# Kernel tuning notes

Measured on AMD Instinct MI355X. Metric: run time of the kernel, lower is better.

Reference implementation:

```python
import jax, jax.numpy as jnp
import numpy as np

N = 40000      # nodes
E = 640000     # edges (avg degree 16)
H = 128        # hidden_dim
D = 4          # propagation_depth
G = 1250       # graphs in batch
T = 32         # target_dim
AF, AV = 9, 64   # atom categorical features, vocab per feature
BF, BV = 3, 8    # bond categorical features, vocab per feature


def silu(x):
    return x * jax.nn.sigmoid(x)


def setup_inputs() -> dict:
    key = jax.random.key(0)
    ks = jax.random.split(key, 32)
    s = 1.0 / np.sqrt(H)

    def w(i, shp, scale):
        return (jax.random.normal(ks[i], shp, jnp.float32) * scale).astype(jnp.float32)

    inp = {}
    inp["atom_feat"] = jax.random.randint(ks[0], (N, AF), 0, AV)
    inp["bond_feat"] = jax.random.randint(ks[1], (E, BF), 0, BV)
    inp["edge_src"] = jax.random.randint(ks[2], (E,), 0, N)
    inp["edge_dst"] = jax.random.randint(ks[3], (E,), 0, N)
    inp["node2graph"] = jnp.sort(jax.random.randint(ks[4], (N,), 0, G))

    inp["atom_emb"] = w(5, (AF, AV, H), 0.1)
    inp["bond_emb"] = w(6, (BF, BV, H), 0.1)
    # message MLP: Linear(3H,H)+SiLU, Linear(H,H)+SiLU (last_activation=mid_activation)
    inp["msg_W1"] = w(7, (D, 3 * H, H), 1.0 / np.sqrt(3 * H))
    inp["msg_b1"] = jnp.zeros((D, H), jnp.float32)
    inp["msg_W2"] = w(8, (D, H, H), s)
    inp["msg_b2"] = jnp.zeros((D, H), jnp.float32)
    # soft edge gate: Linear(H,1) + sigmoid
    inp["gate_W"] = w(9, (D, H, 1), s)
    inp["gate_b"] = jnp.zeros((D, 1), jnp.float32)
    # update MLP: Linear(H,H)+SiLU, Linear(H,H) (last None)
    inp["upd_W1"] = w(10, (D, H, H), s)
    inp["upd_b1"] = jnp.zeros((D, H), jnp.float32)
    inp["upd_W2"] = w(11, (D, H, H), s)
    inp["upd_b2"] = jnp.zeros((D, H), jnp.float32)
    # node_wise_output: Linear(H,H)+SiLU, Linear(H,H) (last None)
    inp["out_W1"] = w(12, (H, H), s)
    inp["out_b1"] = jnp.zeros((H,), jnp.float32)
    inp["out_W2"] = w(13, (H, H), s)
    inp["out_b2"] = jnp.zeros((H,), jnp.float32)
    # readout output MLP: Linear(3H,H)+ReLU, Linear(H,T) (last None)
    inp["ro_W1"] = w(14, (3 * H, H), 1.0 / np.sqrt(3 * H))
    inp["ro_b1"] = jnp.zeros((H,), jnp.float32)
    inp["ro_W2"] = w(15, (H, T), s)
    inp["ro_b2"] = jnp.zeros((T,), jnp.float32)
    return inp


def _forward(atom_feat, bond_feat, edge_src, edge_dst, node2graph,
             atom_emb, bond_emb,
             msg_W1, msg_b1, msg_W2, msg_b2, gate_W, gate_b,
             upd_W1, upd_b1, upd_W2, upd_b2,
             out_W1, out_b1, out_W2, out_b2,
             ro_W1, ro_b1, ro_W2, ro_b2):
    # Atom/Bond encoders: sum of per-feature categorical embeddings
    h = atom_emb[jnp.arange(AF), atom_feat].sum(axis=1)        # [N, H]
    e = bond_emb[jnp.arange(BF), bond_feat].sum(axis=1)        # [E, H]

    for l in range(D):
        src = h[edge_src]                                      # [E, H]
        dst = h[edge_dst]                                      # [E, H]
        m_in = jnp.concatenate([src, dst, e], axis=-1)         # [E, 3H]
        m = silu(silu(m_in @ msg_W1[l] + msg_b1[l]) @ msg_W2[l] + msg_b2[l])
        gate = jax.nn.sigmoid(m @ gate_W[l] + gate_b[l])       # [E, 1]
        m = m * gate
        m_sum = jax.ops.segment_sum(m, edge_dst, num_segments=N)  # [N, H]
        u_in = m_sum + h
        h_new = silu(u_in @ upd_W1[l] + upd_b1[l]) @ upd_W2[l] + upd_b2[l]
        h = h_new + h

    # node-wise output network
    h = silu(h @ out_W1 + out_b1) @ out_W2 + out_b2            # [N, H]

    # per-graph readouts: sum / mean / max
    sums = jax.ops.segment_sum(h, node2graph, num_segments=G)  # [G, H]
    cnt = jax.ops.segment_sum(jnp.ones((N, 1), h.dtype), node2graph, num_segments=G)
    mean = sums / jnp.maximum(cnt, 1.0)
    mx = jax.ops.segment_max(h, node2graph, num_segments=G)
    mx = jnp.where(cnt > 0, mx, 0.0)
    readout = jnp.concatenate([sums, mean, mx], axis=-1)       # [G, 3H]

    return jax.nn.relu(readout @ ro_W1 + ro_b1) @ ro_W2 + ro_b2  # [G, T]


def reference(atom_feat, bond_feat, edge_src, edge_dst, node2graph,
              atom_emb, bond_emb,
              msg_W1, msg_b1, msg_W2, msg_b2, gate_W, gate_b,
              upd_W1, upd_b1, upd_W2, upd_b2,
              out_W1, out_b1, out_W2, out_b2,
              ro_W1, ro_b1, ro_W2, ro_b2):
    return _forward(atom_feat, bond_feat, edge_src, edge_dst, node2graph,
                    atom_emb, bond_emb,
                    msg_W1, msg_b1, msg_W2, msg_b2, gate_W, gate_b,
                    upd_W1, upd_b1, upd_W2, upd_b2,
                    out_W1, out_b1, out_W2, out_b2,
                    ro_W1, ro_b1, ro_W2, ro_b2)
```

## Files before the change

kernel.cpp:

```cpp
#include <hip/hip_runtime.h>
#include <hip/hip_bf16.h>
#include <hip/hip_fp16.h>

#define NN 40000
#define NE 640000
#define HD 128
#define DEPTH 4
#define NG 1250
#define TD 32
#define AFN 9
#define AVN 64
#define BFN 3
#define BVN 8
#define NBLK2 (NE / 128)

typedef short bf16x8 __attribute__((ext_vector_type(8)));
typedef _Float16 f16x8 __attribute__((ext_vector_type(8)));
typedef _Float16 f16x2 __attribute__((ext_vector_type(2)));
typedef float f32x4 __attribute__((ext_vector_type(4)));

__device__ __forceinline__ uint cvtpk(float lo, float hi){
  uint r; asm("v_cvt_pk_bf16_f32 %0, %1, %2" : "=v"(r) : "v"(lo), "v"(hi)); return r;
}
__device__ __forceinline__ ushort f2bf(float x){ return (ushort)cvtpk(x, x); }
__device__ __forceinline__ float rcpfa(float x){ return __builtin_amdgcn_rcpf(x); }
__device__ __forceinline__ float siluf(float x){ return x * rcpfa(1.f + __expf(-x)); }
__device__ __forceinline__ float sigmf(float x){ return rcpfa(1.f + __expf(-x)); }
__device__ __forceinline__ uint packbf2(float a, float b){ return cvtpk(a, b); }

__device__ __forceinline__ __half2 silu_h2(__half2 x){
  const __half2 nl2e = __float2half2_rn(-1.44269504f);
  const __half2 one  = __float2half2_rn(1.f);
  __half2 e = h2exp2(__hmul2(x, nl2e));
  return __hmul2(x, h2rcp(__hadd2(one, e)));
}
union H2U { __half2 h; f16x2 v; uint u; };
__device__ __forceinline__ __half2 pkrtz(float lo, float hi){
  auto t = __builtin_amdgcn_cvt_pkrtz(lo, hi);
  H2U r; __builtin_memcpy(&r.u, &t, 4); return r.h;
}

__device__ __forceinline__ void pack_one(const float* __restrict__ src,
                                         ushort* __restrict__ dst,
                                         int K, int L, int isf16){
  int total = L * K * HD;
  for (int idx = blockIdx.x * blockDim.x + threadIdx.x; idx < total;
       idx += gridDim.x * blockDim.x){
    int l = idx / (K * HD);
    int r = idx - l * K * HD;
    int k = r / HD;
    int n = r - k * HD;
    float v = src[idx];
    ushort o;
    if (isf16){ __half hv = __float2half_rn(v); o = *(ushort*)&hv; }
    else o = f2bf(v);
    dst[(size_t)l * K * HD + ((size_t)(k >> 3) * HD + n) * 8 + (k & 7)] = o;
  }
}
__global__ void pack6(const float* s0, const float* s1, const float* s2,
                      const float* s3, const float* s4, const float* s5,
                      ushort* d0, ushort* d1, ushort* d2,
                      ushort* d3, ushort* d4, ushort* d5){
  switch (blockIdx.y){
    case 0: pack_one(s0, d0, 384, DEPTH, 0); break;
    case 1: pack_one(s1, d1, HD, DEPTH, 1); break;
    case 2: pack_one(s2, d2, HD, DEPTH, 0); break;
    case 3: pack_one(s3, d3, HD, DEPTH, 0); break;
    case 4: pack_one(s4, d4, HD, 1, 0); break;
    default: pack_one(s5, d5, HD, 1, 0); break;
  }
}

__global__ void zero_i(int* __restrict__ p, int n){
  for (int i = blockIdx.x * blockDim.x + threadIdx.x; i < n; i += gridDim.x * blockDim.x)
    p[i] = 0;
}

__global__ void atom_encode(const int* __restrict__ feat, const float* __restrict__ emb,
                            float* __restrict__ h, ushort* __restrict__ hbf){
  int n = blockIdx.x;
  int c = threadIdx.x;
  float acc = 0.f;
#pragma unroll
  for (int f = 0; f < AFN; ++f){
    int v = feat[n * AFN + f];
    acc += emb[(size_t)(f * AVN + v) * HD + c];
  }
  h[(size_t)n * HD + c] = acc;
  hbf[(size_t)n * HD + c] = f2bf(acc);
}

__global__ void ebf_k(const float* __restrict__ bemb, ushort* __restrict__ ebf){
  const int cid = blockIdx.x;
  const int c = threadIdx.x;
  const int f0 = cid >> 6, f1 = (cid >> 3) & 7, f2 = cid & 7;
  float v = bemb[(size_t)(0 * BVN + f0) * HD + c]
          + bemb[(size_t)(1 * BVN + f1) * HD + c]
          + bemb[(size_t)(2 * BVN + f2) * HD + c];
  ebf[(size_t)cid * HD + c] = f2bf(v);
}

__global__ void hist_k(const int* __restrict__ edst, int* __restrict__ deg){
  for (int e = blockIdx.x * blockDim.x + threadIdx.x; e < NE; e += gridDim.x * blockDim.x)
    atomicAdd(&deg[edst[e]], 1);
}

__global__ __launch_bounds__(1024) void scan_head(const int* __restrict__ deg,
                                                  int* __restrict__ head){
  __shared__ int buf[1024];
  const int t = threadIdx.x;
  const int base = t * 40;
  int s = 0;
  int dloc[40];
  if (t < 1000){
#pragma unroll
    for (int i = 0; i < 40; ++i){ dloc[i] = deg[base + i]; s += dloc[i]; }
  }
  buf[t] = s;
  __syncthreads();
  for (int ofs = 1; ofs < 1024; ofs <<= 1){
    int x = (t >= ofs) ? buf[t - ofs] : 0;
    __syncthreads();
    buf[t] += x;
    __syncthreads();
  }
  if (t < 1000){
    int run = buf[t] - s;
#pragma unroll
    for (int i = 0; i < 40; ++i){ head[base + i] = run; run += dloc[i]; }
  }
}

__global__ void scatter_k(const int* __restrict__ esrc, const int* __restrict__ edst,
                          const int* __restrict__ bfeat, int* __restrict__ head,
                          int* __restrict__ esrc_p, int* __restrict__ dst_p,
                          int* __restrict__ cid_p){
  for (int e = blockIdx.x * blockDim.x + threadIdx.x; e < NE; e += gridDim.x * blockDim.x){
    const int d = edst[e];
    const int pos = atomicAdd(&head[d], 1);
    esrc_p[pos] = esrc[e];
    dst_p[pos] = d;
    cid_p[pos] = bfeat[e * 3 + 0] * 64 + bfeat[e * 3 + 1] * 8 + bfeat[e * 3 + 2];
  }
}

__global__ __launch_bounds__(256) void pre_k(
    const ushort* __restrict__ hbf, const ushort* __restrict__ W1p,
    __half* __restrict__ prea, __half* __restrict__ preb,
    float* __restrict__ msum)
{
  const int tid = threadIdx.x;
  const int n0 = blockIdx.x * 64;
  {
    const float4 z = make_float4(0.f, 0.f, 0.f, 0.f);
    float4* mz = (float4*)(msum + (size_t)n0 * HD);
#pragma unroll
    for (int i = 0; i < 8; ++i) mz[tid + i * 256] = z;
  }
  const int lane = tid & 63, wv = tid >> 6;
  const int lr = lane & 15, lg = lane >> 4;
  const int arow = n0 + wv * 16 + lr;
  bf16x8 a[4];
#pragma unroll
  for (int ks = 0; ks < 4; ++ks)
    a[ks] = *(const bf16x8*)(hbf + (size_t)arow * HD + ks * 32 + lg * 8);
  const f32x4 zero = {0.f, 0.f, 0.f, 0.f};
  f32x4 acc[16];
#pragma unroll
  for (int i = 0; i < 16; ++i) acc[i] = zero;
#pragma unroll
  for (int ks = 0; ks < 4; ++ks){
#pragma unroll
    for (int ct = 0; ct < 16; ++ct){
      const int oct = ks * 4 + lg + ((ct >= 8) ? 16 : 0);
      const int ncol = (ct & 7) * 16 + lr;
      bf16x8 b = *(const bf16x8*)(W1p + ((size_t)oct * HD + ncol) * 8);
      acc[ct] = __builtin_amdgcn_mfma_f32_16x16x32_bf16(a[ks], b, acc[ct], 0, 0, 0);
    }
  }
#pragma unroll
  for (int ct = 0; ct < 16; ++ct){
    __half* dstp = (ct < 8) ? prea : preb;
    const int ncol = (ct & 7) * 16 + lr;
#pragma unroll
    for (int r = 0; r < 4; ++r){
      const int nrow = n0 + wv * 16 + lg * 4 + r;
      dstp[(size_t)nrow * HD + ncol] = __float2half_rn(acc[ct][r]);
    }
  }
}

__global__ __launch_bounds__(256) void ew1c_k(
    const ushort* __restrict__ ebf, const ushort* __restrict__ W1p_all,
    const float* __restrict__ b1_all, __half* __restrict__ ecb_all)
{
  const int l = blockIdx.y;
  const ushort* W1p = W1p_all + (size_t)l * 384 * HD;
  const float* b1v = b1_all + l * HD;
  __half* ecb = ecb_all + (size_t)l * 512 * HD;
  const int tid = threadIdx.x;
  const int c0 = blockIdx.x * 64;
  const int lane = tid & 63, wv = tid >> 6;
  const int lr = lane & 15, lg = lane >> 4;
  const int arow = c0 + wv * 16 + lr;
  bf16x8 a[4];
#pragma unroll
  for (int ks = 0; ks < 4; ++ks)
    a[ks] = *(const bf16x8*)(ebf + (size_t)arow * HD + ks * 32 + lg * 8);
  const f32x4 zero = {0.f, 0.f, 0.f, 0.f};
  f32x4 acc[8];
#pragma unroll
  for (int i = 0; i < 8; ++i) acc[i] = zero;
#pragma unroll
  for (int ks = 0; ks < 4; ++ks){
#pragma unroll
    for (int ct = 0; ct < 8; ++ct){
      const int oct = ks * 4 + lg + 32;
      const int ncol = ct * 16 + lr;
      bf16x8 b = *(const bf16x8*)(W1p + ((size_t)oct * HD + ncol) * 8);
      acc[ct] = __builtin_amdgcn_mfma_f32_16x16x32_bf16(a[ks], b, acc[ct], 0, 0, 0);
    }
  }
#pragma unroll
  for (int ct = 0; ct < 8; ++ct){
    const int ncol = ct * 16 + lr;
    const float bias = b1v[ncol];
#pragma unroll
    for (int r = 0; r < 4; ++r){
      const int nrow = c0 + wv * 16 + lg * 4 + r;
      ecb[(size_t)nrow * HD + ncol] = __float2half_rn(acc[ct][r] + bias);
    }
  }
}

__device__ __forceinline__ void build_af(
    const __half* __restrict__ prea, const __half* __restrict__ preb,
    const __half* __restrict__ ecb, int s, int d, int c, int lg, f16x8* af)
{
#pragma unroll
  for (int ks = 0; ks < 4; ++ks){
    const int off = ks * 32 + lg * 8;
    union { uint4 q; __half2 h[4]; f16x8 v; } ua, ub, uc, uo;
    ua.q = *(const uint4*)(prea + (size_t)s * HD + off);
    ub.q = *(const uint4*)(preb + (size_t)d * HD + off);
    uc.q = *(const uint4*)(ecb + (size_t)c * HD + off);
#pragma unroll
    for (int j = 0; j < 4; ++j)
      uo.h[j] = silu_h2(__hadd2(__hadd2(ua.h[j], ub.h[j]), uc.h[j]));
    af[ks] = uo.v;
  }
}

__device__ __forceinline__ void edge_epilogue(
    f32x4* acc, int lr, int lg, int rowbase,
    const float* b2l, const float* b2h, const __half2* gwh, float gbias,
    uint* Ms)
{
  __half2 mh[4][4];
#pragma unroll
  for (int ct = 0; ct < 4; ++ct){
#pragma unroll
    for (int r = 0; r < 4; ++r)
      mh[ct][r] = silu_h2(pkrtz(acc[ct][r] + b2l[ct], acc[ct + 4][r] + b2h[ct]));
  }
#pragma unroll
  for (int r = 0; r < 4; ++r){
    float sgs = 0.f;
#pragma unroll
    for (int ct = 0; ct < 4; ++ct){
      H2U a, b; a.h = mh[ct][r]; b.h = gwh[ct];
      sgs = __builtin_amdgcn_fdot2(a.v, b.v, sgs, false);
    }
    sgs += __shfl_xor(sgs, 1); sgs += __shfl_xor(sgs, 2);
    sgs += __shfl_xor(sgs, 4); sgs += __shfl_xor(sgs, 8);
    const __half2 gh = __float2half2_rn(sigmf(sgs + gbias));
#pragma unroll
    for (int ct = 0; ct < 4; ++ct) mh[ct][r] = __hmul2(mh[ct][r], gh);
  }
#pragma unroll
  for (int ct = 0; ct < 4; ++ct){
    const int ui = ct * 16 + lr;
#pragma unroll
    for (int r = 0; r < 4; ++r){
      const int lrow = rowbase + lg * 4 + r;
      H2U w; w.h = mh[ct][r];
      *(uint*)((char*)Ms + lrow * 256 + (((uint)(ui * 4)) ^ ((uint)((lrow & 7) << 4)))) = w.u;
    }
  }
}

__global__ __launch_bounds__(256, 4) void msg2_kernel(
    const __half* __restrict__ prea, const __half* __restrict__ preb,
    const __half* __restrict__ ecb,
    const int* __restrict__ esrc_p, const int* __restrict__ dst_p,
    const int* __restrict__ cid_p,
    const __half* __restrict__ W2p, const float* __restrict__ b2v,
    const float* __restrict__ gw, const float* __restrict__ gb,
    float* __restrict__ msum)
{
  __shared__ uint Ms[128 * 64];
  __shared__ int dsh[128];
  const int tid = threadIdx.x;
  const int bid = (int)blockIdx.x;
  const int bsw = (bid & 7) * (NBLK2 >> 3) + (bid >> 3);
  const int e0 = bsw * 128;
  if (tid < 128) dsh[tid] = dst_p[e0 + tid];

  const int lane = tid & 63;
  const int wv = tid >> 6;
  const int lr = lane & 15, lg = lane >> 4;
  const int row0 = e0 + wv * 16 + lr;
  const int row1 = row0 + 64;
  const int s0 = esrc_p[row0], d0 = dst_p[row0], c0 = cid_p[row0];
  const int s1 = esrc_p[row1], d1 = dst_p[row1], c1 = cid_p[row1];

  f16x8 af0[4], af1[4];
  build_af(prea, preb, ecb, s0, d0, c0, lg, af0);
  build_af(prea, preb, ecb, s1, d1, c1, lg, af1);

  const f32x4 zero = {0.f, 0.f, 0.f, 0.f};
  f32x4 acc0[8], acc1[8];
#pragma unroll
  for (int i = 0; i < 8; ++i){ acc0[i] = zero; acc1[i] = zero; }
#pragma unroll
  for (int ks = 0; ks < 4; ++ks){
    const __half* wb = W2p + ((size_t)(ks * 4 + lg) * HD + lr) * 8;
#pragma unroll
    for (int ct = 0; ct < 8; ++ct){
      f16x8 b = *(const f16x8*)(wb + ct * 16 * 8);
      acc0[ct] = __builtin_amdgcn_mfma_f32_16x16x32_f16(af0[ks], b, acc0[ct], 0, 0, 0);
      acc1[ct] = __builtin_amdgcn_mfma_f32_16x16x32_f16(af1[ks], b, acc1[ct], 0, 0, 0);
    }
  }

  float b2l[4], b2h[4];
  __half2 gwh[4];
#pragma unroll
  for (int ct = 0; ct < 4; ++ct){
    b2l[ct] = b2v[ct * 16 + lr];
    b2h[ct] = b2v[ct * 16 + lr + 64];
    gwh[ct] = pkrtz(gw[ct * 16 + lr], gw[ct * 16 + lr + 64]);
  }
  const float gbias = gb[0];
  edge_epilogue(acc0, lr, lg, wv * 16, b2l, b2h, gwh, gbias, Ms);
  edge_epilogue(acc1, lr, lg, 64 + wv * 16, b2l, b2h, gwh, gbias, Ms);
  __syncthreads();

  {
    const int cp = tid & 63;
    const int seg = tid >> 6;
    const int r0 = seg * 32, r1 = r0 + 32;
    float rl = 0.f, rh = 0.f;
    int cur = dsh[r0];
    for (int r = r0; r < r1; ++r){
      const int dd = dsh[r];
      if (dd != cur){
        atomicAdd(&msum[(size_t)cur * HD + cp], rl);
        atomicAdd(&msum[(size_t)cur * HD + cp + 64], rh);
        rl = 0.f; rh = 0.f; cur = dd;
      }
      H2U w;
      w.u = *(const uint*)((const char*)Ms + r * 256 +
                           (((uint)(cp * 4)) ^ ((uint)((r & 7) << 4))));
      rl += __low2float(w.h); rh += __high2float(w.h);
    }
    atomicAdd(&msum[(size_t)cur * HD + cp], rl);
    atomicAdd(&msum[(size_t)cur * HD + cp + 64], rh);
  }
}

template <int MODE>
__global__ __launch_bounds__(256) void node_mlp(
    const float* hin, const float* __restrict__ msum,
    const ushort* __restrict__ W1p, const ushort* __restrict__ W2p,
    const float* __restrict__ b1v, const float* __restrict__ b2v,
    float* outp, ushort* __restrict__ hbf)
{
  __shared__ ushort At[64 * 128];
  __shared__ ushort Tt[64 * 128];
  const int tid = threadIdx.x;
  const int n0 = blockIdx.x * 64;

  {
    const int nl = tid >> 2, part = tid & 3;
    const int node = n0 + nl;
    const float4* hp = (const float4*)(hin + (size_t)node * HD + part * 32);
    const float4* mp = (MODE == 0) ? (const float4*)(msum + (size_t)node * HD + part * 32) : nullptr;
    char* rowp = (char*)At + nl * 256;
    const uint sw = (uint)((nl & 7) << 4);
#pragma unroll
    for (int j = 0; j < 4; ++j){
      float4 x0 = hp[j * 2 + 0], x1 = hp[j * 2 + 1];
      if (MODE == 0){
        float4 m0 = mp[j * 2 + 0], m1 = mp[j * 2 + 1];
        x0.x += m0.x; x0.y += m0.y; x0.z += m0.z; x0.w += m0.w;
        x1.x += m1.x; x1.y += m1.y; x1.z += m1.z; x1.w += m1.w;
      }
      uint4 o;
      o.x = packbf2(x0.x, x0.y); o.y = packbf2(x0.z, x0.w);
      o.z = packbf2(x1.x, x1.y); o.w = packbf2(x1.z, x1.w);
      uint cb = (uint)(part * 64 + j * 16);
      *(uint4*)(rowp + (cb ^ sw)) = o;
    }
  }
  __syncthreads();

  const int lane = tid & 63;
  const int wv = tid >> 6;
  const int lr = lane & 15, lg = lane >> 4;
  const int rowbase = wv * 16;
  const f32x4 zero = {0.f, 0.f, 0.f, 0.f};
  const int arow = rowbase + lr;
  const char* arp = (const char*)At + arow * 256;
  const uint asw = (uint)((arow & 7) << 4);

  f32x4 acc[8];
#pragma unroll
  for (int i = 0; i < 8; ++i) acc[i] = zero;
#pragma unroll
  for (int ks = 0; ks < 4; ++ks){
    uint cb = (uint)(ks * 64 + lg * 16);
    bf16x8 a = *(const bf16x8*)(arp + (cb ^ asw));
    const ushort* wbase = W1p + ((size_t)(ks * 4 + lg) * 128 + lr) * 8;
#pragma unroll
    for (int ct = 0; ct < 8; ++ct){
      bf16x8 b = *(const bf16x8*)(wbase + ct * 16 * 8);
      acc[ct] = __builtin_amdgcn_mfma_f32_16x16x32_bf16(a, b, acc[ct], 0, 0, 0);
    }
  }
#pragma unroll
  for (int ct = 0; ct < 8; ++ct){
    const int col = ct * 16 + lr;
    const float bias = b1v[col];
#pragma unroll
    for (int r = 0; r < 4; ++r){
      const int row = rowbase + lg * 4 + r;
      float v = siluf(acc[ct][r] + bias);
      *(ushort*)((char*)Tt + row * 256 + (((uint)(col * 2)) ^ ((uint)(row & 7) << 4))) = f2bf(v);
    }
  }
  __syncthreads();

  f32x4 acc2[8];
#pragma unroll
  for (int i = 0; i < 8; ++i) acc2[i] = zero;
  {
    const char* trp = (const char*)Tt + arow * 256;
#pragma unroll
    for (int ks = 0; ks < 4; ++ks){
      uint cb = (uint)(ks * 64 + lg * 16);
      bf16x8 a = *(const bf16x8*)(trp + (cb ^ asw));
      const ushort* wbase = W2p + ((size_t)(ks * 4 + lg) * 128 + lr) * 8;
#pragma unroll
      for (int ct = 0; ct < 8; ++ct){
        bf16x8 b = *(const bf16x8*)(wbase + ct * 16 * 8);
        acc2[ct] = __builtin_amdgcn_mfma_f32_16x16x32_bf16(a, b, acc2[ct], 0, 0, 0);
      }
    }
  }
#pragma unroll
  for (int ct = 0; ct < 8; ++ct){
    const int col = ct * 16 + lr;
    const float bias = b2v[col];
#pragma unroll
    for (int r = 0; r < 4; ++r){
      const int node = n0 + rowbase + lg * 4 + r;
      float v = acc2[ct][r] + bias;
      if (MODE == 0) v += hin[(size_t)node * HD + col];
      outp[(size_t)node * HD + col] = v;
      if (MODE == 0) hbf[(size_t)node * HD + col] = f2bf(v);
    }
  }
}

__global__ __launch_bounds__(128) void readout_final(
    const float* __restrict__ hout, const int* __restrict__ n2g,
    const float* __restrict__ W1, const float* __restrict__ b1,
    const float* __restrict__ W2, const float* __restrict__ b2,
    float* __restrict__ out){
  __shared__ float rsh[384];
  __shared__ float hr[128];
  const int g = blockIdx.x;
  const int c = threadIdx.x;
  int lo, hi;
  { int a = 0, b = NN; while (a < b){ int mid = (a + b) >> 1; if (n2g[mid] < g) a = mid + 1; else b = mid; } lo = a; }
  { int a = lo, b = NN; while (a < b){ int mid = (a + b) >> 1; if (n2g[mid] < g + 1) a = mid + 1; else b = mid; } hi = a; }
  float s = 0.f, mx = -3.4e38f;
  for (int n = lo; n < hi; ++n){
    float v = hout[(size_t)n * HD + c];
    s += v; mx = fmaxf(mx, v);
  }
  const int cnt = hi - lo;
  float mean = (cnt > 0) ? s / (float)cnt : 0.f;
  if (cnt == 0){ s = 0.f; mx = 0.f; }
  rsh[c] = s; rsh[128 + c] = mean; rsh[256 + c] = mx;
  __syncthreads();
  float acc = b1[c];
#pragma unroll 4
  for (int j = 0; j < 384; ++j) acc += rsh[j] * W1[j * 128 + c];
  hr[c] = fmaxf(acc, 0.f);
  __syncthreads();
  if (c < TD){
    float o = b2[c];
#pragma unroll 4
    for (int j = 0; j < 128; ++j) o += hr[j] * W2[j * TD + c];
    out[(size_t)g * TD + c] = o;
  }
}

extern "C" void kernel_launch(void* const* d_in, const int* in_sizes, int n_in,
                              void* d_out, int out_size, void* d_ws, size_t ws_size,
                              hipStream_t stream)
{
  const int*   atom_feat  = (const int*)  d_in[0];
  const int*   bond_feat  = (const int*)  d_in[1];
  const int*   edge_src   = (const int*)  d_in[2];
  const int*   edge_dst   = (const int*)  d_in[3];
  const int*   node2graph = (const int*)  d_in[4];
  const float* atom_emb   = (const float*)d_in[5];
  const float* bond_emb   = (const float*)d_in[6];
  const float* msg_W1     = (const float*)d_in[7];
  const float* msg_b1     = (const float*)d_in[8];
  const float* msg_W2     = (const float*)d_in[9];
  const float* msg_b2     = (const float*)d_in[10];
  const float* gate_W     = (const float*)d_in[11];
  const float* gate_b     = (const float*)d_in[12];
  const float* upd_W1     = (const float*)d_in[13];
  const float* upd_b1     = (const float*)d_in[14];
  const float* upd_W2     = (const float*)d_in[15];
  const float* upd_b2     = (const float*)d_in[16];
  const float* out_W1     = (const float*)d_in[17];
  const float* out_b1     = (const float*)d_in[18];
  const float* out_W2     = (const float*)d_in[19];
  const float* out_b2     = (const float*)d_in[20];
  const float* ro_W1      = (const float*)d_in[21];
  const float* ro_b1      = (const float*)d_in[22];
  const float* ro_W2      = (const float*)d_in[23];
  const float* ro_b2      = (const float*)d_in[24];
  (void)in_sizes; (void)n_in; (void)out_size; (void)ws_size;

  char* ws = (char*)d_ws;
  size_t off = 0;
  auto alloc = [&](size_t bytes) -> char* {
    char* p = ws + off;
    off = (off + bytes + 255) & ~(size_t)255;
    return p;
  };
  float*  h      = (float*) alloc((size_t)NN * HD * 4);
  ushort* hbf    = (ushort*)alloc((size_t)NN * HD * 2);
  float*  msum   = (float*) alloc((size_t)NN * HD * 4);
  ushort* msgW1p = (ushort*)alloc((size_t)DEPTH * 384 * HD * 2);
  ushort* msgW2p = (ushort*)alloc((size_t)DEPTH * HD * HD * 2);
  ushort* updW1p = (ushort*)alloc((size_t)DEPTH * HD * HD * 2);
  ushort* updW2p = (ushort*)alloc((size_t)DEPTH * HD * HD * 2);
  ushort* outW1p = (ushort*)alloc((size_t)HD * HD * 2);
  ushort* outW2p = (ushort*)alloc((size_t)HD * HD * 2);
  ushort* ebf    = (ushort*)alloc((size_t)512 * HD * 2);
  __half* ecb    = (__half*)alloc((size_t)DEPTH * 512 * HD * 2);
  __half* prea   = (__half*)alloc((size_t)NN * HD * 2);
  __half* preb   = (__half*)alloc((size_t)NN * HD * 2);
  int*    deg    = (int*)   alloc((size_t)NN * 4);
  int*    head   = (int*)   alloc((size_t)NN * 4);
  int*    esrc_p = (int*)   alloc((size_t)NE * 4);
  int*    dst_p  = (int*)   alloc((size_t)NE * 4);
  int*    cid_p  = (int*)   alloc((size_t)NE * 4);
  float*  hout   = msum;

  pack6<<<dim3(48, 6), 256, 0, stream>>>(msg_W1, msg_W2, upd_W1, upd_W2, out_W1, out_W2,
                                         msgW1p, msgW2p, updW1p, updW2p, outW1p, outW2p);
  atom_encode<<<NN, HD, 0, stream>>>(atom_feat, atom_emb, h, hbf);
  ebf_k<<<512, HD, 0, stream>>>(bond_emb, ebf);
  ew1c_k<<<dim3(8, DEPTH), 256, 0, stream>>>(ebf, msgW1p, msg_b1, ecb);

  zero_i<<<160, 256, 0, stream>>>(deg, NN);
  hist_k<<<640, 256, 0, stream>>>(edge_dst, deg);
  scan_head<<<1, 1024, 0, stream>>>(deg, head);
  scatter_k<<<640, 256, 0, stream>>>(edge_src, edge_dst, bond_feat, head,
                                     esrc_p, dst_p, cid_p);

  for (int l = 0; l < DEPTH; ++l){
    pre_k<<<NN / 64, 256, 0, stream>>>(hbf, msgW1p + (size_t)l * 384 * HD, prea, preb, msum);
    msg2_kernel<<<NBLK2, 256, 0, stream>>>(
        prea, preb, ecb + (size_t)l * 512 * HD,
        esrc_p, dst_p, cid_p,
        (const __half*)msgW2p + (size_t)l * HD * HD,
        msg_b2 + l * HD, gate_W + l * HD, gate_b + l, msum);
    node_mlp<0><<<NN / 64, 256, 0, stream>>>(
        h, msum,
        updW1p + (size_t)l * HD * HD, updW2p + (size_t)l * HD * HD,
        upd_b1 + l * HD, upd_b2 + l * HD, h, hbf);
  }
  node_mlp<1><<<NN / 64, 256, 0, stream>>>(
      h, nullptr, outW1p, outW2p, out_b1, out_b2, hout, nullptr);
  readout_final<<<NG, 128, 0, stream>>>(hout, node2graph, ro_W1, ro_b1, ro_W2, ro_b2,
                                        (float*)d_out);
}
```

Before: 710.6 us.

## Fuse edge messaging, aggregation and node update into one per-node-block kernel

Replaces the per-edge-block message kernel plus separate node MLP with a kernel that owns 64 destination nodes, walks their dst-sorted edge range, computes gated messages, and accumulates them into an LDS buffer with shared atomics instead of global atomics. The update MLP then runs in the same block, reading the aggregated messages from LDS, which removes the global msum array, its zeroing, and a kernel launch per layer. Edge metadata is packed into one int (bond class plus local dst offset), dropping a per-edge index array. In exchange, per-block work is uneven because edge counts per 64-node block vary, and partial 64-row tiles waste MFMA work.

Result: slower. 1.320 ms (+85.8%).

```diff
diff --git a/kernel.cpp b/kernel.cpp
--- a/kernel.cpp
+++ b/kernel.cpp
@@ -12,7 +12,7 @@
 #define AVN 64
 #define BFN 3
 #define BVN 8
-#define NBLK2 (NE / 128)
+#define MROW 132
 
 typedef short bf16x8 __attribute__((ext_vector_type(8)));
 typedef _Float16 f16x8 __attribute__((ext_vector_type(8)));
@@ -133,30 +133,22 @@
 
 __global__ void scatter_k(const int* __restrict__ esrc, const int* __restrict__ edst,
                           const int* __restrict__ bfeat, int* __restrict__ head,
-                          int* __restrict__ esrc_p, int* __restrict__ dst_p,
-                          int* __restrict__ cid_p){
+                          int* __restrict__ esrc_p, int* __restrict__ pc_p){
   for (int e = blockIdx.x * blockDim.x + threadIdx.x; e < NE; e += gridDim.x * blockDim.x){
     const int d = edst[e];
     const int pos = atomicAdd(&head[d], 1);
+    const int cid = bfeat[e * 3 + 0] * 64 + bfeat[e * 3 + 1] * 8 + bfeat[e * 3 + 2];
     esrc_p[pos] = esrc[e];
-    dst_p[pos] = d;
-    cid_p[pos] = bfeat[e * 3 + 0] * 64 + bfeat[e * 3 + 1] * 8 + bfeat[e * 3 + 2];
+    pc_p[pos] = (cid << 6) | (d & 63);
   }
 }
 
 __global__ __launch_bounds__(256) void pre_k(
     const ushort* __restrict__ hbf, const ushort* __restrict__ W1p,
-    __half* __restrict__ prea, __half* __restrict__ preb,
-    float* __restrict__ msum)
+    __half* __restrict__ prea, __half* __restrict__ preb)
 {
   const int tid = threadIdx.x;
   const int n0 = blockIdx.x * 64;
-  {
-    const float4 z = make_float4(0.f, 0.f, 0.f, 0.f);
-    float4* mz = (float4*)(msum + (size_t)n0 * HD);
-#pragma unroll
-    for (int i = 0; i < 8; ++i) mz[tid + i * 256] = z;
-  }
   const int lane = tid & 63, wv = tid >> 6;
   const int lr = lane & 15, lg = lane >> 4;
   const int arow = n0 + wv * 16 + lr;
@@ -251,12 +243,11 @@
   }
 }
 
-__device__ __forceinline__ void edge_epilogue(
-    f32x4* acc, int lr, int lg, int rowbase,
+__device__ __forceinline__ void edge_epilogue_r(
+    const f32x4* acc, int lr,
     const float* b2l, const float* b2h, const __half2* gwh, float gbias,
-    uint* Ms)
-{
-  __half2 mh[4][4];
+    __half2 mh[4][4])
+{
 #pragma unroll
   for (int ct = 0; ct < 4; ++ct){
 #pragma unroll
@@ -277,61 +268,64 @@
 #pragma unroll
     for (int ct = 0; ct < 4; ++ct) mh[ct][r] = __hmul2(mh[ct][r], gh);
   }
+}
+
+__device__ __forceinline__ void accum_seg(
+    __half2 mh[4][4], int rowbase, int hi,
+    const int* __restrict__ pc_p, int lr, int lg, float* __restrict__ Msum)
+{
+  const int rb = rowbase + lg * 4;
+  int dl[4]; bool val[4];
+#pragma unroll
+  for (int r = 0; r < 4; ++r){
+    const int rr = rb + r;
+    val[r] = rr < hi;
+    dl[r] = pc_p[min(rr, hi - 1)] & 63;
+  }
 #pragma unroll
   for (int ct = 0; ct < 4; ++ct){
-    const int ui = ct * 16 + lr;
-#pragma unroll
-    for (int r = 0; r < 4; ++r){
-      const int lrow = rowbase + lg * 4 + r;
-      H2U w; w.h = mh[ct][r];
-      *(uint*)((char*)Ms + lrow * 256 + (((uint)(ui * 4)) ^ ((uint)((lrow & 7) << 4)))) = w.u;
-    }
-  }
-}
-
-__global__ __launch_bounds__(256, 4) void msg2_kernel(
+    const int cp = ct * 16 + lr;
+    __half2 s = mh[ct][0];
+    int cur = dl[0]; bool sv = val[0];
+#pragma unroll
+    for (int r = 1; r < 4; ++r){
+      if (val[r] && sv && dl[r] == cur){
+        s = __hadd2(s, mh[ct][r]);
+      } else {
+        if (sv){
+          atomicAdd(&Msum[cur * MROW + cp], __low2float(s));
+          atomicAdd(&Msum[cur * MROW + cp + 64], __high2float(s));
+        }
+        s = mh[ct][r]; cur = dl[r]; sv = val[r];
+      }
+    }
+    if (sv){
+      atomicAdd(&Msum[cur * MROW + cp], __low2float(s));
+      atomicAdd(&Msum[cur * MROW + cp + 64], __high2float(s));
+    }
+  }
+}
+
+__global__ __launch_bounds__(256, 4) void mega_kernel(
     const __half* __restrict__ prea, const __half* __restrict__ preb,
     const __half* __restrict__ ecb,
-    const int* __restrict__ esrc_p, const int* __restrict__ dst_p,
-    const int* __restrict__ cid_p,
+    const int* __restrict__ esrc_p, const int* __restrict__ pc_p,
+    const int* __restrict__ eend,
     const __half* __restrict__ W2p, const float* __restrict__ b2v,
     const float* __restrict__ gw, const float* __restrict__ gb,
-    float* __restrict__ msum)
-{
-  __shared__ uint Ms[128 * 64];
-  __shared__ int dsh[128];
+    const ushort* __restrict__ uW1p, const ushort* __restrict__ uW2p,
+    const float* __restrict__ ub1, const float* __restrict__ ub2,
+    float* __restrict__ h, ushort* __restrict__ hbf)
+{
+  __shared__ float Msum[64 * MROW];
   const int tid = threadIdx.x;
-  const int bid = (int)blockIdx.x;
-  const int bsw = (bid & 7) * (NBLK2 >> 3) + (bid >> 3);
-  const int e0 = bsw * 128;
-  if (tid < 128) dsh[tid] = dst_p[e0 + tid];
-
-  const int lane = tid & 63;
-  const int wv = tid >> 6;
+  const int lane = tid & 63, wv = tid >> 6;
   const int lr = lane & 15, lg = lane >> 4;
-  const int row0 = e0 + wv * 16 + lr;
-  const int row1 = row0 + 64;
-  const int s0 = esrc_p[row0], d0 = dst_p[row0], c0 = cid_p[row0];
-  const int s1 = esrc_p[row1], d1 = dst_p[row1], c1 = cid_p[row1];
-
-  f16x8 af0[4], af1[4];
-  build_af(prea, preb, ecb, s0, d0, c0, lg, af0);
-  build_af(prea, preb, ecb, s1, d1, c1, lg, af1);
-
-  const f32x4 zero = {0.f, 0.f, 0.f, 0.f};
-  f32x4 acc0[8], acc1[8];
-#pragma unroll
-  for (int i = 0; i < 8; ++i){ acc0[i] = zero; acc1[i] = zero; }
-#pragma unroll
-  for (int ks = 0; ks < 4; ++ks){
-    const __half* wb = W2p + ((size_t)(ks * 4 + lg) * HD + lr) * 8;
-#pragma unroll
-    for (int ct = 0; ct < 8; ++ct){
-      f16x8 b = *(const f16x8*)(wb + ct * 16 * 8);
-      acc0[ct] = __builtin_amdgcn_mfma_f32_16x16x32_f16(af0[ks], b, acc0[ct], 0, 0, 0);
-      acc1[ct] = __builtin_amdgcn_mfma_f32_16x16x32_f16(af1[ks], b, acc1[ct], 0, 0, 0);
-    }
-  }
+  const int n0 = (int)blockIdx.x * 64;
+  const int lo = (n0 == 0) ? 0 : eend[n0 - 1];
+  const int hi = eend[n0 + 63];
+
+  for (int i = tid; i < 64 * MROW; i += 256) Msum[i] = 0.f;
 
   float b2l[4], b2h[4];
   __half2 gwh[4];
@@ -342,60 +336,156 @@
     gwh[ct] = pkrtz(gw[ct * 16 + lr], gw[ct * 16 + lr + 64]);
   }
   const float gbias = gb[0];
-  edge_epilogue(acc0, lr, lg, wv * 16, b2l, b2h, gwh, gbias, Ms);
-  edge_epilogue(acc1, lr, lg, 64 + wv * 16, b2l, b2h, gwh, gbias, Ms);
-  __syncthreads();
-
+  __syncthreads();
+
+  const f32x4 zero = {0.f, 0.f, 0.f, 0.f};
+
+  for (int t = lo; t < hi; t += 128){
+    const bool two = (t + 64) < hi;
+    const int rowA0 = t + wv * 16 + lr;
+    f16x8 af0[4], af1[4];
+    {
+      const int ra = min(rowA0, hi - 1);
+      const int s = esrc_p[ra], pc = pc_p[ra];
+      build_af(prea, preb, ecb, s, n0 + (pc & 63), pc >> 6, lg, af0);
+    }
+    if (two){
+      const int ra = min(rowA0 + 64, hi - 1);
+      const int s = esrc_p[ra], pc = pc_p[ra];
+      build_af(prea, preb, ecb, s, n0 + (pc & 63), pc >> 6, lg, af1);
+    }
+    f32x4 acc0[8], acc1[8];
+#pragma unroll
+    for (int i = 0; i < 8; ++i){ acc0[i] = zero; acc1[i] = zero; }
+    if (two){
+#pragma unroll
+      for (int ks = 0; ks < 4; ++ks){
+        const __half* wb = W2p + ((size_t)(ks * 4 + lg) * HD + lr) * 8;
+#pragma unroll
+        for (int ct = 0; ct < 8; ++ct){
+          f16x8 b = *(const f16x8*)(wb + ct * 16 * 8);
+          acc0[ct] = __builtin_amdgcn_mfma_f32_16x16x32_f16(af0[ks], b, acc0[ct], 0, 0, 0);
+          acc1[ct] = __builtin_amdgcn_mfma_f32_16x16x32_f16(af1[ks], b, acc1[ct], 0, 0, 0);
+        }
+      }
+    } else {
+#pragma unroll
+      for (int ks = 0; ks < 4; ++ks){
+        const __half* wb = W2p + ((size_t)(ks * 4 + lg) * HD + lr) * 8;
+#pragma unroll
+        for (int ct = 0; ct < 8; ++ct){
+          f16x8 b = *(const f16x8*)(wb + ct * 16 * 8);
+          acc0[ct] = __builtin_amdgcn_mfma_f32_16x16x32_f16(af0[ks], b, acc0[ct], 0, 0, 0);
+        }
+      }
+    }
+    __half2 mh[4][4];
+    edge_epilogue_r(acc0, lr, b2l, b2h, gwh, gbias, mh);
+    accum_seg(mh, t + wv * 16, hi, pc_p, lr, lg, Msum);
+    if (two){
+      edge_epilogue_r(acc1, lr, b2l, b2h, gwh, gbias, mh);
+      accum_seg(mh, t + 64 + wv * 16, hi, pc_p, lr, lg, Msum);
+    }
+  }
+  __syncthreads();
+
+  const int arow = wv * 16 + lr;
+  bf16x8 au[4];
+#pragma unroll
+  for (int ks = 0; ks < 4; ++ks){
+    const int k0 = ks * 32 + lg * 8;
+    const float* mp = &Msum[arow * MROW + k0];
+    float4 m0 = *(const float4*)mp;
+    float4 m1 = *(const float4*)(mp + 4);
+    const float* hp = &h[(size_t)(n0 + arow) * HD + k0];
+    float4 h0 = *(const float4*)hp;
+    float4 h1 = *(const float4*)(hp + 4);
+    uint4 o;
+    o.x = packbf2(m0.x + h0.x, m0.y + h0.y);
+    o.y = packbf2(m0.z + h0.z, m0.w + h0.w);
+    o.z = packbf2(m1.x + h1.x, m1.y + h1.y);
+    o.w = packbf2(m1.z + h1.z, m1.w + h1.w);
+    __builtin_memcpy(&au[ks], &o, 16);
+  }
+  __syncthreads();
+
+  ushort* Tt = (ushort*)Msum;
+  f32x4 uacc[8];
+#pragma unroll
+  for (int i = 0; i < 8; ++i) uacc[i] = zero;
+#pragma unroll
+  for (int ks = 0; ks < 4; ++ks){
+    const ushort* wbase = uW1p + ((size_t)(ks * 4 + lg) * HD + lr) * 8;
+#pragma unroll
+    for (int ct = 0; ct < 8; ++ct){
+      bf16x8 b = *(const bf16x8*)(wbase + ct * 16 * 8);
+      uacc[ct] = __builtin_amdgcn_mfma_f32_16x16x32_bf16(au[ks], b, uacc[ct], 0, 0, 0);
+    }
+  }
+#pragma unroll
+  for (int ct = 0; ct < 8; ++ct){
+    const int col = ct * 16 + lr;
+    const float bias = ub1[col];
+#pragma unroll
+    for (int r = 0; r < 4; ++r){
+      const int row = wv * 16 + lg * 4 + r;
+      float v = siluf(uacc[ct][r] + bias);
+      *(ushort*)((char*)Tt + row * 256 + (((uint)(col * 2)) ^ ((uint)((row & 7) << 4)))) = f2bf(v);
+    }
+  }
+  __syncthreads();
+
+  f32x4 uacc2[8];
+#pragma unroll
+  for (int i = 0; i < 8; ++i) uacc2[i] = zero;
   {
-    const int cp = tid & 63;
-    const int seg = tid >> 6;
-    const int r0 = seg * 32, r1 = r0 + 32;
-    float rl = 0.f, rh = 0.f;
-    int cur = dsh[r0];
-    for (int r = r0; r < r1; ++r){
-      const int dd = dsh[r];
-      if (dd != cur){
-        atomicAdd(&msum[(size_t)cur * HD + cp], rl);
-        atomicAdd(&msum[(size_t)cur * HD + cp + 64], rh);
-        rl = 0.f; rh = 0.f; cur = dd;
+    const char* trp = (const char*)Tt + arow * 256;
+    const uint asw = (uint)((arow & 7) << 4);
+#pragma unroll
+    for (int ks = 0; ks < 4; ++ks){
+      uint cb = (uint)(ks * 64 + lg * 16);
+      bf16x8 a = *(const bf16x8*)(trp + (cb ^ asw));
+      const ushort* wbase = uW2p + ((size_t)(ks * 4 + lg) * HD + lr) * 8;
+#pragma unroll
+      for (int ct = 0; ct < 8; ++ct){
+        bf16x8 b = *(const bf16x8*)(wbase + ct * 16 * 8);
+        uacc2[ct] = __builtin_amdgcn_mfma_f32_16x16x32_bf16(a, b, uacc2[ct], 0, 0, 0);
       }
-      H2U w;
-      w.u = *(const uint*)((const char*)Ms + r * 256 +
-                           (((uint)(cp * 4)) ^ ((uint)((r & 7) << 4))));
-      rl += __low2float(w.h); rh += __high2float(w.h);
-    }
-    atomicAdd(&msum[(size_t)cur * HD + cp], rl);
-    atomicAdd(&msum[(size_t)cur * HD + cp + 64], rh);
-  }
-}
-
-template <int MODE>
-__global__ __launch_bounds__(256) void node_mlp(
-    const float* hin, const float* __restrict__ msum,
+    }
+  }
+#pragma unroll
+  for (int ct = 0; ct < 8; ++ct){
+    const int col = ct * 16 + lr;
+    const float bias = ub2[col];
+#pragma unroll
+    for (int r = 0; r < 4; ++r){
+      const int node = n0 + wv * 16 + lg * 4 + r;
+      float v = uacc2[ct][r] + bias + h[(size_t)node * HD + col];
+      h[(size_t)node * HD + col] = v;
+      hbf[(size_t)node * HD + col] = f2bf(v);
+    }
+  }
+}
+
+__global__ __launch_bounds__(256) void node_out(
+    const float* __restrict__ hin,
     const ushort* __restrict__ W1p, const ushort* __restrict__ W2p,
     const float* __restrict__ b1v, const float* __restrict__ b2v,
-    float* outp, ushort* __restrict__ hbf)
+    float* __restrict__ outp)
 {
   __shared__ ushort At[64 * 128];
   __shared__ ushort Tt[64 * 128];
   const int tid = threadIdx.x;
   const int n0 = blockIdx.x * 64;
-
   {
     const int nl = tid >> 2, part = tid & 3;
     const int node = n0 + nl;
     const float4* hp = (const float4*)(hin + (size_t)node * HD + part * 32);
-    const float4* mp = (MODE == 0) ? (const float4*)(msum + (size_t)node * HD + part * 32) : nullptr;
     char* rowp = (char*)At + nl * 256;
     const uint sw = (uint)((nl & 7) << 4);
 #pragma unroll
     for (int j = 0; j < 4; ++j){
       float4 x0 = hp[j * 2 + 0], x1 = hp[j * 2 + 1];
-      if (MODE == 0){
-        float4 m0 = mp[j * 2 + 0], m1 = mp[j * 2 + 1];
-        x0.x += m0.x; x0.y += m0.y; x0.z += m0.z; x0.w += m0.w;
-        x1.x += m1.x; x1.y += m1.y; x1.z += m1.z; x1.w += m1.w;
-      }
       uint4 o;
       o.x = packbf2(x0.x, x0.y); o.y = packbf2(x0.z, x0.w);
       o.z = packbf2(x1.x, x1.y); o.w = packbf2(x1.z, x1.w);
@@ -404,16 +494,12 @@
     }
   }
   __syncthreads();
-
-  const int lane = tid & 63;
-  const int wv = tid >> 6;
+  const int lane = tid & 63, wv = tid >> 6;
   const int lr = lane & 15, lg = lane >> 4;
-  const int rowbase = wv * 16;
   const f32x4 zero = {0.f, 0.f, 0.f, 0.f};
-  const int arow = rowbase + lr;
+  const int arow = wv * 16 + lr;
   const char* arp = (const char*)At + arow * 256;
   const uint asw = (uint)((arow & 7) << 4);
-
   f32x4 acc[8];
 #pragma unroll
   for (int i = 0; i < 8; ++i) acc[i] = zero;
@@ -421,7 +507,7 @@
   for (int ks = 0; ks < 4; ++ks){
     uint cb = (uint)(ks * 64 + lg * 16);
     bf16x8 a = *(const bf16x8*)(arp + (cb ^ asw));
-    const ushort* wbase = W1p + ((size_t)(ks * 4 + lg) * 128 + lr) * 8;
+    const ushort* wbase = W1p + ((size_t)(ks * 4 + lg) * HD + lr) * 8;
 #pragma unroll
     for (int ct = 0; ct < 8; ++ct){
       bf16x8 b = *(const bf16x8*)(wbase + ct * 16 * 8);
@@ -434,13 +520,12 @@
     const float bias = b1v[col];
 #pragma unroll
     for (int r = 0; r < 4; ++r){
-      const int row = rowbase + lg * 4 + r;
+      const int row = wv * 16 + lg * 4 + r;
       float v = siluf(acc[ct][r] + bias);
       *(ushort*)((char*)Tt + row * 256 + (((uint)(col * 2)) ^ ((uint)(row & 7) << 4))) = f2bf(v);
     }
   }
   __syncthreads();
-
   f32x4 acc2[8];
 #pragma unroll
   for (int i = 0; i < 8; ++i) acc2[i] = zero;
@@ -450,7 +535,7 @@
     for (int ks = 0; ks < 4; ++ks){
       uint cb = (uint)(ks * 64 + lg * 16);
       bf16x8 a = *(const bf16x8*)(trp + (cb ^ asw));
-      const ushort* wbase = W2p + ((size_t)(ks * 4 + lg) * 128 + lr) * 8;
+      const ushort* wbase = W2p + ((size_t)(ks * 4 + lg) * HD + lr) * 8;
 #pragma unroll
       for (int ct = 0; ct < 8; ++ct){
         bf16x8 b = *(const bf16x8*)(wbase + ct * 16 * 8);
@@ -464,11 +549,8 @@
     const float bias = b2v[col];
 #pragma unroll
     for (int r = 0; r < 4; ++r){
-      const int node = n0 + rowbase + lg * 4 + r;
-      float v = acc2[ct][r] + bias;
-      if (MODE == 0) v += hin[(size_t)node * HD + col];
-      outp[(size_t)node * HD + col] = v;
-      if (MODE == 0) hbf[(size_t)node * HD + col] = f2bf(v);
+      const int node = n0 + wv * 16 + lg * 4 + r;
+      outp[(size_t)node * HD + col] = acc2[ct][r] + bias;
     }
   }
 }
@@ -547,8 +629,8 @@
     return p;
   };
   float*  h      = (float*) alloc((size_t)NN * HD * 4);
+  float*  hout   = (float*) alloc((size_t)NN * HD * 4);
   ushort* hbf    = (ushort*)alloc((size_t)NN * HD * 2);
-  float*  msum   = (float*) alloc((size_t)NN * HD * 4);
   ushort* msgW1p = (ushort*)alloc((size_t)DEPTH * 384 * HD * 2);
   ushort* msgW2p = (ushort*)alloc((size_t)DEPTH * HD * HD * 2);
   ushort* updW1p = (ushort*)alloc((size_t)DEPTH * HD * HD * 2);
@@ -562,9 +644,7 @@
   int*    deg    = (int*)   alloc((size_t)NN * 4);
   int*    head   = (int*)   alloc((size_t)NN * 4);
   int*    esrc_p = (int*)   alloc((size_t)NE * 4);
-  int*    dst_p  = (int*)   alloc((size_t)NE * 4);
-  int*    cid_p  = (int*)   alloc((size_t)NE * 4);
-  float*  hout   = msum;
+  int*    pc_p   = (int*)   alloc((size_t)NE * 4);
 
   pack6<<<dim3(48, 6), 256, 0, stream>>>(msg_W1, msg_W2, upd_W1, upd_W2, out_W1, out_W2,
                                          msgW1p, msgW2p, updW1p, updW2p, outW1p, outW2p);
@@ -576,22 +656,20 @@
   hist_k<<<640, 256, 0, stream>>>(edge_dst, deg);
   scan_head<<<1, 1024, 0, stream>>>(deg, head);
   scatter_k<<<640, 256, 0, stream>>>(edge_src, edge_dst, bond_feat, head,
-                                     esrc_p, dst_p, cid_p);
+                                     esrc_p, pc_p);
 
   for (int l = 0; l < DEPTH; ++l){
-    pre_k<<<NN / 64, 256, 0, stream>>>(hbf, msgW1p + (size_t)l * 384 * HD, prea, preb, msum);
-    msg2_kernel<<<NBLK2, 256, 0, stream>>>(
+    pre_k<<<NN / 64, 256, 0, stream>>>(hbf, msgW1p + (size_t)l * 384 * HD, prea, preb);
+    mega_kernel<<<NN / 64, 256, 0, stream>>>(
         prea, preb, ecb + (size_t)l * 512 * HD,
-        esrc_p, dst_p, cid_p,
+        esrc_p, pc_p, head,
         (const __half*)msgW2p + (size_t)l * HD * HD,
-        msg_b2 + l * HD, gate_W + l * HD, gate_b + l, msum);
-    node_mlp<0><<<NN / 64, 256, 0, stream>>>(
-        h, msum,
+        msg_b2 + l * HD, gate_W + l * HD, gate_b + l,
         updW1p + (size_t)l * HD * HD, updW2p + (size_t)l * HD * HD,
-        upd_b1 + l * HD, upd_b2 + l * HD, h, hbf);
-  }
-  node_mlp<1><<<NN / 64, 256, 0, stream>>>(
-      h, nullptr, outW1p, outW2p, out_b1, out_b2, hout, nullptr);
+        upd_b1 + l * HD, upd_b2 + l * HD,
+        h, hbf);
+  }
+  node_out<<<NN / 64, 256, 0, stream>>>(h, outW1p, outW2p, out_b1, out_b2, hout);
   readout_final<<<NG, 128, 0, stream>>>(hout, node2graph, ro_W1, ro_b1, ro_W2, ro_b2,
                                         (float*)d_out);
 }
```

## Process 128 nodes per block in node_mlp with register-loaded A tiles

Applied to the files above, without the earlier changes.

Each node_mlp block now handles two 64-row tiles, so every weight fragment loaded from global memory feeds two MFMAs. The first-layer input is converted to bf16 and kept in registers, which drops the shared-memory A buffer and one barrier. A partial last tile is guarded by a validity flag, and launch bounds now ask for 4 blocks per CU. In exchange the kernel uses more registers and half as many blocks are launched.

Result: slower. 754.4 us (+6.2%).

```diff
diff --git a/kernel.cpp b/kernel.cpp
--- a/kernel.cpp
+++ b/kernel.cpp
@@ -370,62 +370,67 @@
 }
 
 template <int MODE>
-__global__ __launch_bounds__(256) void node_mlp(
+__global__ __launch_bounds__(256, 4) void node_mlp(
     const float* hin, const float* __restrict__ msum,
     const ushort* __restrict__ W1p, const ushort* __restrict__ W2p,
     const float* __restrict__ b1v, const float* __restrict__ b2v,
     float* outp, ushort* __restrict__ hbf)
 {
-  __shared__ ushort At[64 * 128];
-  __shared__ ushort Tt[64 * 128];
+  __shared__ ushort Tt[128 * 128];
   const int tid = threadIdx.x;
-  const int n0 = blockIdx.x * 64;
-
-  {
-    const int nl = tid >> 2, part = tid & 3;
-    const int node = n0 + nl;
-    const float4* hp = (const float4*)(hin + (size_t)node * HD + part * 32);
-    const float4* mp = (MODE == 0) ? (const float4*)(msum + (size_t)node * HD + part * 32) : nullptr;
-    char* rowp = (char*)At + nl * 256;
-    const uint sw = (uint)((nl & 7) << 4);
-#pragma unroll
-    for (int j = 0; j < 4; ++j){
-      float4 x0 = hp[j * 2 + 0], x1 = hp[j * 2 + 1];
+  const int lane = tid & 63, wv = tid >> 6;
+  const int lr = lane & 15, lg = lane >> 4;
+  const int n0 = (int)blockIdx.x * 128;
+  const int row0 = wv * 16 + lr;
+  const bool t1v = (n0 + 64) < NN;
+  const int nrow1 = t1v ? (n0 + 64 + row0) : (n0 + row0);
+
+  bf16x8 a0[4], a1[4];
+#pragma unroll
+  for (int ks = 0; ks < 4; ++ks){
+    const int k0 = ks * 32 + lg * 8;
+    {
+      const float* hp = hin + (size_t)(n0 + row0) * HD + k0;
+      float4 h0 = *(const float4*)hp, h1 = *(const float4*)(hp + 4);
       if (MODE == 0){
-        float4 m0 = mp[j * 2 + 0], m1 = mp[j * 2 + 1];
-        x0.x += m0.x; x0.y += m0.y; x0.z += m0.z; x0.w += m0.w;
-        x1.x += m1.x; x1.y += m1.y; x1.z += m1.z; x1.w += m1.w;
+        const float* mp = msum + (size_t)(n0 + row0) * HD + k0;
+        float4 m0 = *(const float4*)mp, m1 = *(const float4*)(mp + 4);
+        h0.x += m0.x; h0.y += m0.y; h0.z += m0.z; h0.w += m0.w;
+        h1.x += m1.x; h1.y += m1.y; h1.z += m1.z; h1.w += m1.w;
       }
       uint4 o;
-      o.x = packbf2(x0.x, x0.y); o.y = packbf2(x0.z, x0.w);
-      o.z = packbf2(x1.x, x1.y); o.w = packbf2(x1.z, x1.w);
-      uint cb = (uint)(part * 64 + j * 16);
-      *(uint4*)(rowp + (cb ^ sw)) = o;
-    }
-  }
-  __syncthreads();
-
-  const int lane = tid & 63;
-  const int wv = tid >> 6;
-  const int lr = lane & 15, lg = lane >> 4;
-  const int rowbase = wv * 16;
+      o.x = packbf2(h0.x, h0.y); o.y = packbf2(h0.z, h0.w);
+      o.z = packbf2(h1.x, h1.y); o.w = packbf2(h1.z, h1.w);
+      __builtin_memcpy(&a0[ks], &o, 16);
+    }
+    {
+      const float* hp = hin + (size_t)nrow1 * HD + k0;
+      float4 h0 = *(const float4*)hp, h1 = *(const float4*)(hp + 4);
+      if (MODE == 0){
+        const float* mp = msum + (size_t)nrow1 * HD + k0;
+        float4 m0 = *(const float4*)mp, m1 = *(const float4*)(mp + 4);
+        h0.x += m0.x; h0.y += m0.y; h0.z += m0.z; h0.w += m0.w;
+        h1.x += m1.x; h1.y += m1.y; h1.z += m1.z; h1.w += m1.w;
+      }
+      uint4 o;
+      o.x = packbf2(h0.x, h0.y); o.y = packbf2(h0.z, h0.w);
+      o.z = packbf2(h1.x, h1.y); o.w = packbf2(h1.z, h1.w);
+      __builtin_memcpy(&a1[ks], &o, 16);
+    }
+  }
+
   const f32x4 zero = {0.f, 0.f, 0.f, 0.f};
-  const int arow = rowbase + lr;
-  const char* arp = (const char*)At + arow * 256;
-  const uint asw = (uint)((arow & 7) << 4);
-
-  f32x4 acc[8];
-#pragma unroll
-  for (int i = 0; i < 8; ++i) acc[i] = zero;
+  f32x4 acc0[8], acc1[8];
+#pragma unroll
+  for (int i = 0; i < 8; ++i){ acc0[i] = zero; acc1[i] = zero; }
 #pragma unroll
   for (int ks = 0; ks < 4; ++ks){
-    uint cb = (uint)(ks * 64 + lg * 16);
-    bf16x8 a = *(const bf16x8*)(arp + (cb ^ asw));
-    const ushort* wbase = W1p + ((size_t)(ks * 4 + lg) * 128 + lr) * 8;
+    const ushort* wbase = W1p + ((size_t)(ks * 4 + lg) * HD + lr) * 8;
 #pragma unroll
     for (int ct = 0; ct < 8; ++ct){
       bf16x8 b = *(const bf16x8*)(wbase + ct * 16 * 8);
-      acc[ct] = __builtin_amdgcn_mfma_f32_16x16x32_bf16(a, b, acc[ct], 0, 0, 0);
+      acc0[ct] = __builtin_amdgcn_mfma_f32_16x16x32_bf16(a0[ks], b, acc0[ct], 0, 0, 0);
+      acc1[ct] = __builtin_amdgcn_mfma_f32_16x16x32_bf16(a1[ks], b, acc1[ct], 0, 0, 0);
     }
   }
 #pragma unroll
@@ -434,27 +439,34 @@
     const float bias = b1v[col];
 #pragma unroll
     for (int r = 0; r < 4; ++r){
-      const int row = rowbase + lg * 4 + r;
-      float v = siluf(acc[ct][r] + bias);
-      *(ushort*)((char*)Tt + row * 256 + (((uint)(col * 2)) ^ ((uint)(row & 7) << 4))) = f2bf(v);
+      const int rw0 = wv * 16 + lg * 4 + r;
+      float v0 = siluf(acc0[ct][r] + bias);
+      *(ushort*)((char*)Tt + rw0 * 256 + (((uint)(col * 2)) ^ ((uint)((rw0 & 7) << 4)))) = f2bf(v0);
+      const int rw1 = rw0 + 64;
+      float v1 = siluf(acc1[ct][r] + bias);
+      *(ushort*)((char*)Tt + rw1 * 256 + (((uint)(col * 2)) ^ ((uint)((rw1 & 7) << 4)))) = f2bf(v1);
     }
   }
   __syncthreads();
 
-  f32x4 acc2[8];
-#pragma unroll
-  for (int i = 0; i < 8; ++i) acc2[i] = zero;
+#pragma unroll
+  for (int i = 0; i < 8; ++i){ acc0[i] = zero; acc1[i] = zero; }
   {
-    const char* trp = (const char*)Tt + arow * 256;
+    const char* trp0 = (const char*)Tt + row0 * 256;
+    const char* trp1 = (const char*)Tt + (row0 + 64) * 256;
+    const uint asw0 = (uint)((row0 & 7) << 4);
+    const uint asw1 = (uint)(((row0 + 64) & 7) << 4);
 #pragma unroll
     for (int ks = 0; ks < 4; ++ks){
       uint cb = (uint)(ks * 64 + lg * 16);
-      bf16x8 a = *(const bf16x8*)(trp + (cb ^ asw));
-      const ushort* wbase = W2p + ((size_t)(ks * 4 + lg) * 128 + lr) * 8;
+      bf16x8 ta0 = *(const bf16x8*)(trp0 + (cb ^ asw0));
+      bf16x8 ta1 = *(const bf16x8*)(trp1 + (cb ^ asw1));
+      const ushort* wbase = W2p + ((size_t)(ks * 4 + lg) * HD + lr) * 8;
 #pragma unroll
       for (int ct = 0; ct < 8; ++ct){
         bf16x8 b = *(const bf16x8*)(wbase + ct * 16 * 8);
-        acc2[ct] = __builtin_amdgcn_mfma_f32_16x16x32_bf16(a, b, acc2[ct], 0, 0, 0);
+        acc0[ct] = __builtin_amdgcn_mfma_f32_16x16x32_bf16(ta0, b, acc0[ct], 0, 0, 0);
+        acc1[ct] = __builtin_amdgcn_mfma_f32_16x16x32_bf16(ta1, b, acc1[ct], 0, 0, 0);
       }
     }
   }
@@ -464,11 +476,18 @@
     const float bias = b2v[col];
 #pragma unroll
     for (int r = 0; r < 4; ++r){
-      const int node = n0 + rowbase + lg * 4 + r;
-      float v = acc2[ct][r] + bias;
-      if (MODE == 0) v += hin[(size_t)node * HD + col];
-      outp[(size_t)node * HD + col] = v;
-      if (MODE == 0) hbf[(size_t)node * HD + col] = f2bf(v);
+      const int node0 = n0 + wv * 16 + lg * 4 + r;
+      float v0 = acc0[ct][r] + bias;
+      if (MODE == 0) v0 += hin[(size_t)node0 * HD + col];
+      outp[(size_t)node0 * HD + col] = v0;
+      if (MODE == 0) hbf[(size_t)node0 * HD + col] = f2bf(v0);
+      if (t1v){
+        const int node1 = node0 + 64;
+        float v1 = acc1[ct][r] + bias;
+        if (MODE == 0) v1 += hin[(size_t)node1 * HD + col];
+        outp[(size_t)node1 * HD + col] = v1;
+        if (MODE == 0) hbf[(size_t)node1 * HD + col] = f2bf(v1);
+      }
     }
   }
 }
@@ -585,12 +604,12 @@
         esrc_p, dst_p, cid_p,
         (const __half*)msgW2p + (size_t)l * HD * HD,
         msg_b2 + l * HD, gate_W + l * HD, gate_b + l, msum);
-    node_mlp<0><<<NN / 64, 256, 0, stream>>>(
+    node_mlp<0><<<(NN + 127) / 128, 256, 0, stream>>>(
         h, msum,
         updW1p + (size_t)l * HD * HD, updW2p + (size_t)l * HD * HD,
         upd_b1 + l * HD, upd_b2 + l * HD, h, hbf);
   }
-  node_mlp<1><<<NN / 64, 256, 0, stream>>>(
+  node_mlp<1><<<(NN + 127) / 128, 256, 0, stream>>>(
       h, nullptr, outW1p, outW2p, out_b1, out_b2, hout, nullptr);
   readout_final<<<NG, 128, 0, stream>>>(hout, node2graph, ro_W1, ro_b1, ro_W2, ro_b2,
                                         (float*)d_out);
```
